# Performance work log

Hardware: AMD Instinct MI355X
Metric: run time of the kernel (lower is better)

The kernel has to match this reference:

```python
import jax, jax.numpy as jnp
import numpy as np

IN_F, OUT_F, USER_F = 1024, 512, 512
BSZ, S = 64, 256


def setup_inputs() -> dict:
    key = jax.random.key(0)
    k = jax.random.split(key, 7)
    X_doc = jax.random.normal(k[0], (BSZ, S, IN_F), dtype=jnp.float32)
    X_user = jax.random.normal(k[1], (BSZ, S, USER_F), dtype=jnp.float32)
    # xavier-normal-ish scaling for weights
    Wd = jax.random.normal(k[2], (OUT_F, IN_F), dtype=jnp.float32) * np.sqrt(2.0 / (IN_F + OUT_F))
    bd = jnp.zeros((OUT_F,), dtype=jnp.float32)
    Wu = jax.random.normal(k[3], (OUT_F, USER_F), dtype=jnp.float32) * np.sqrt(2.0 / (USER_F + OUT_F))
    bu = jnp.zeros((OUT_F,), dtype=jnp.float32)
    W = jax.random.normal(k[4], (OUT_F, OUT_F), dtype=jnp.float32) * np.sqrt(1.0 / OUT_F)
    return {"X_doc": X_doc, "X_user": X_user, "Wd": Wd, "bd": bd, "Wu": Wu, "bu": bu, "W": W}


def reference(X_doc, X_user, Wd, bd, Wu, bu, W):
    d = jnp.einsum('bsi,oi->bso', X_doc, Wd) + bd          # (b, s, out)
    u = jnp.einsum('bsi,oi->bso', X_user, Wu) + bu          # (b, s, out)
    d = d * jax.nn.sigmoid(u)
    u = u * jax.nn.sigmoid(d)
    att = jnp.tanh(jnp.einsum('bsd,de,bre->bsr', d, W, u))  # (b, s, s)
    score_d = jax.nn.softmax(att.mean(axis=2), axis=1)[..., None]  # (b, s, 1)
    score_u = jax.nn.softmax(att.mean(axis=1), axis=1)[..., None]  # (b, s, 1)
    attention_d = jnp.sum(score_d * d, axis=1)              # (b, out)
    attention_u = jnp.sum(score_u * u, axis=1)              # (b, out)
    return (attention_d, attention_u)
```

## Files before the change

### kernel.cpp

```cpp
#include <hip/hip_runtime.h>

#define S_ 256
#define BSZ_ 64
#define IN_F_ 1024
#define OUT_F_ 512
#define USER_F_ 512

typedef short short8 __attribute__((ext_vector_type(8)));
typedef float f32x4 __attribute__((ext_vector_type(4)));

__device__ __forceinline__ ushort f2bf(float f) {
  unsigned u = __float_as_uint(f);
  unsigned r = (u + 0x7FFFu + ((u >> 16) & 1u)) >> 16;
  return (ushort)r;
}
__device__ __forceinline__ float bf2f(unsigned hi16) {
  return __uint_as_float(hi16 << 16);
}
__device__ __forceinline__ float sigf(float x) {
  return 1.f / (1.f + __expf(-x));
}
__device__ __forceinline__ float tanh_safe(float x) {
  float ax = fabsf(x);
  float e = __expf(-2.f * ax);
  float r = (1.f - e) / (1.f + e);
  return copysignf(r, x);
}

__device__ __forceinline__ void gl_lds16(const ushort* g, ushort* l) {
  __builtin_amdgcn_global_load_lds(
      (const __attribute__((address_space(1))) void*)g,
      (__attribute__((address_space(3))) void*)l, 16, 0, 0);
}

__global__ void convert_bf16(const float* __restrict__ in, ushort* __restrict__ out, long n) {
  long i = ((long)blockIdx.x * blockDim.x + threadIdx.x) * 4;
  if (i + 3 < n) {
    float4 v = *(const float4*)(in + i);
    ushort4 o;
    o.x = f2bf(v.x); o.y = f2bf(v.y); o.z = f2bf(v.z); o.w = f2bf(v.w);
    *(ushort4*)(out + i) = o;
  }
}

__global__ void convert_transpose_w(const float* __restrict__ in, ushort* __restrict__ out) {
  int i = blockIdx.x * blockDim.x + threadIdx.x;
  int e = i >> 9, d = i & 511;
  out[i] = f2bf(in[d * 512 + e]);
}

__global__ void zerof(float* __restrict__ p, int n) {
  int i = blockIdx.x * 256 + threadIdx.x;
  if (i < n) p[i] = 0.f;
}

__device__ __forceinline__ void stage_tile(const ushort* __restrict__ g, int K,
                                           ushort* lds, int w, int lane) {
  const int rin = lane >> 3;
  const int c = lane & 7;
#pragma unroll
  for (int i = 0; i < 4; ++i) {
    int r = w * 32 + i * 8 + rin;
    int gc = c ^ (r & 7);
    gl_lds16(g + (long)r * K + gc * 8, lds + w * 2048 + i * 512);
  }
}

__device__ __forceinline__ short8 frag(const ushort* lds, int row, int kk, int q) {
  int pc = (kk * 4 + q) ^ (row & 7);
  return *(const short8*)(lds + row * 64 + pc * 8);
}

__device__ __forceinline__ void compute_step(const ushort* As, const ushort* Bs,
                                             f32x4 acc[4][4], int wr, int wc,
                                             int mlane, int q) {
#pragma unroll
  for (int kk = 0; kk < 2; ++kk) {
    short8 af[4], bfr[4];
#pragma unroll
    for (int r = 0; r < 4; ++r) af[r] = frag(As, wr * 64 + r * 16 + mlane, kk, q);
#pragma unroll
    for (int c = 0; c < 4; ++c) bfr[c] = frag(Bs, wc * 64 + c * 16 + mlane, kk, q);
#pragma unroll
    for (int r = 0; r < 4; ++r)
#pragma unroll
      for (int c = 0; c < 4; ++c)
        acc[r][c] = __builtin_amdgcn_mfma_f32_16x16x32_bf16(af[r], bfr[c], acc[r][c], 0, 0, 0);
  }
}

template <int NSTEP>
__device__ __forceinline__ void gemm_loop(const ushort* __restrict__ A,
                                          const ushort* __restrict__ B, int K,
                                          ushort* As0, ushort* Bs0,
                                          ushort* As1, ushort* Bs1,
                                          f32x4 acc[4][4], int w, int lane,
                                          int wr, int wc, int mlane, int q) {
  stage_tile(A, K, As0, w, lane);
  stage_tile(B, K, Bs0, w, lane);
#pragma unroll 1
  for (int k = 0; k < NSTEP; k += 2) {
    __syncthreads();
    if (k + 1 < NSTEP) {
      stage_tile(A + (k + 1) * 64, K, As1, w, lane);
      stage_tile(B + (k + 1) * 64, K, Bs1, w, lane);
    }
    compute_step(As0, Bs0, acc, wr, wc, mlane, q);
    __syncthreads();
    if (k + 2 < NSTEP) {
      stage_tile(A + (k + 2) * 64, K, As0, w, lane);
      stage_tile(B + (k + 2) * 64, K, Bs0, w, lane);
    }
    if (k + 1 < NSTEP) compute_step(As1, Bs1, acc, wr, wc, mlane, q);
  }
  __syncthreads();
}

#define ACC_ZERO(a)                         \
  _Pragma("unroll") for (int r = 0; r < 4; ++r) \
  _Pragma("unroll") for (int c = 0; c < 4; ++c) { \
    a[r][c][0] = 0.f; a[r][c][1] = 0.f; a[r][c][2] = 0.f; a[r][c][3] = 0.f; }

__global__ __launch_bounds__(256, 2) void gemm_du(
    const ushort* __restrict__ Xd, const ushort* __restrict__ Wd,
    const float* __restrict__ bd,
    const ushort* __restrict__ Xu, const ushort* __restrict__ Wu,
    const float* __restrict__ bu,
    ushort* __restrict__ dg, ushort* __restrict__ ug) {
  __shared__ ushort sm[32768];
  ushort* As0 = sm; ushort* Bs0 = sm + 8192;
  ushort* As1 = sm + 16384; ushort* Bs1 = sm + 24576;
  const int tid = threadIdx.x, lane = tid & 63, w = tid >> 6;
  const int wr = w >> 1, wc = w & 1, mlane = lane & 15, q = lane >> 4;
  const int m0 = blockIdx.y * 128, n0 = blockIdx.x * 128;

  f32x4 accd[4][4]; ACC_ZERO(accd);
  gemm_loop<16>(Xd + (long)m0 * 1024, Wd + (long)n0 * 1024, 1024,
                As0, Bs0, As1, Bs1, accd, w, lane, wr, wc, mlane, q);
  f32x4 accu[4][4]; ACC_ZERO(accu);
  gemm_loop<8>(Xu + (long)m0 * 512, Wu + (long)n0 * 512, 512,
               As0, Bs0, As1, Bs1, accu, w, lane, wr, wc, mlane, q);

#pragma unroll
  for (int c = 0; c < 4; ++c) {
    const int gn = n0 + wc * 64 + c * 16 + mlane;
    const float bdv = bd[gn], buv = bu[gn];
#pragma unroll
    for (int r = 0; r < 4; ++r)
#pragma unroll
      for (int i = 0; i < 4; ++i) {
        const int gm = m0 + wr * 64 + r * 16 + q * 4 + i;
        const long idx = (long)gm * OUT_F_ + gn;
        float dp = accd[r][c][i] + bdv;
        float up = accu[r][c][i] + buv;
        float dgv = dp * sigf(up);
        float ugv = up * sigf(dgv);
        dg[idx] = f2bf(dgv);
        ug[idx] = f2bf(ugv);
      }
  }
}

__global__ __launch_bounds__(256, 2) void gemm_t(
    const ushort* __restrict__ dgp, const ushort* __restrict__ Wt,
    ushort* __restrict__ tout) {
  __shared__ ushort sm[32768];
  ushort* As0 = sm; ushort* Bs0 = sm + 8192;
  ushort* As1 = sm + 16384; ushort* Bs1 = sm + 24576;
  const int tid = threadIdx.x, lane = tid & 63, w = tid >> 6;
  const int wr = w >> 1, wc = w & 1, mlane = lane & 15, q = lane >> 4;
  const int m0 = blockIdx.y * 128, n0 = blockIdx.x * 128;

  f32x4 acc[4][4]; ACC_ZERO(acc);
  gemm_loop<8>(dgp + (long)m0 * 512, Wt + (long)n0 * 512, 512,
               As0, Bs0, As1, Bs1, acc, w, lane, wr, wc, mlane, q);

#pragma unroll
  for (int c = 0; c < 4; ++c) {
    const int gn = n0 + wc * 64 + c * 16 + mlane;
#pragma unroll
    for (int r = 0; r < 4; ++r)
#pragma unroll
      for (int i = 0; i < 4; ++i) {
        const int gm = m0 + wr * 64 + r * 16 + q * 4 + i;
        tout[(long)gm * OUT_F_ + gn] = f2bf(acc[r][c][i]);
      }
  }
}

__global__ __launch_bounds__(256, 2) void gemm_att(
    const ushort* __restrict__ t, const ushort* __restrict__ ug,
    float* __restrict__ rowlog, float* __restrict__ collog) {
  __shared__ ushort sm[32768];
  ushort* As0 = sm; ushort* Bs0 = sm + 8192;
  ushort* As1 = sm + 16384; ushort* Bs1 = sm + 24576;
  const int tid = threadIdx.x, lane = tid & 63, w = tid >> 6;
  const int wr = w >> 1, wc = w & 1, mlane = lane & 15, q = lane >> 4;
  const int b = blockIdx.z;
  const ushort* A = t + (long)b * (S_ * OUT_F_) + (long)blockIdx.y * 128 * 512;
  const ushort* B = ug + (long)b * (S_ * OUT_F_) + (long)blockIdx.x * 128 * 512;

  f32x4 acc[4][4]; ACC_ZERO(acc);
  gemm_loop<8>(A, B, 512, As0, Bs0, As1, Bs1, acc, w, lane, wr, wc, mlane, q);

  float rs[4][4];
  float cs[4];
#pragma unroll
  for (int r = 0; r < 4; ++r)
#pragma unroll
    for (int i = 0; i < 4; ++i) rs[r][i] = 0.f;
#pragma unroll
  for (int c = 0; c < 4; ++c) cs[c] = 0.f;
#pragma unroll
  for (int r = 0; r < 4; ++r)
#pragma unroll
    for (int c = 0; c < 4; ++c)
#pragma unroll
      for (int i = 0; i < 4; ++i) {
        float v = tanh_safe(acc[r][c][i]);
        rs[r][i] += v;
        cs[c] += v;
      }
#pragma unroll
  for (int m = 1; m < 16; m <<= 1)
#pragma unroll
    for (int r = 0; r < 4; ++r)
#pragma unroll
      for (int i = 0; i < 4; ++i) rs[r][i] += __shfl_xor(rs[r][i], m, 64);
#pragma unroll
  for (int m = 16; m < 64; m <<= 1)
#pragma unroll
    for (int c = 0; c < 4; ++c) cs[c] += __shfl_xor(cs[c], m, 64);

  float* rsum = (float*)sm;
  float* csum = ((float*)sm) + 128;
  if (tid < 128) rsum[tid] = 0.f;
  else if (tid < 256) csum[tid - 128] = 0.f;
  __syncthreads();
  if (mlane == 0) {
#pragma unroll
    for (int r = 0; r < 4; ++r)
#pragma unroll
      for (int i = 0; i < 4; ++i)
        atomicAdd(&rsum[wr * 64 + r * 16 + q * 4 + i], rs[r][i]);
  }
  if (q == 0) {
#pragma unroll
    for (int c = 0; c < 4; ++c) atomicAdd(&csum[wc * 64 + c * 16 + mlane], cs[c]);
  }
  __syncthreads();
  if (tid < 128)
    atomicAdd(&rowlog[b * S_ + blockIdx.y * 128 + tid], rsum[tid]);
  else if (tid < 256)
    atomicAdd(&collog[b * S_ + blockIdx.x * 128 + (tid - 128)], csum[tid - 128]);
}

__device__ __forceinline__ float block_max(float v, float* buf, int tid) {
  buf[tid] = v; __syncthreads();
  for (int s = 128; s > 0; s >>= 1) {
    if (tid < s) buf[tid] = fmaxf(buf[tid], buf[tid + s]);
    __syncthreads();
  }
  float r = buf[0]; __syncthreads();
  return r;
}
__device__ __forceinline__ float block_sum(float v, float* buf, int tid) {
  buf[tid] = v; __syncthreads();
  for (int s = 128; s > 0; s >>= 1) {
    if (tid < s) buf[tid] = buf[tid] + buf[tid + s];
    __syncthreads();
  }
  float r = buf[0]; __syncthreads();
  return r;
}

__global__ __launch_bounds__(256) void finalize(
    const float* __restrict__ rowlog, const float* __restrict__ collog,
    const ushort* __restrict__ dg, const ushort* __restrict__ ug,
    float* __restrict__ out) {
  __shared__ float sd[S_], su[S_], buf[S_];
  const int b = blockIdx.x, tid = threadIdx.x;

  const float rowmean = rowlog[b * S_ + tid] * (1.f / (float)S_);
  const float colmean = collog[b * S_ + tid] * (1.f / (float)S_);

  float md = block_max(rowmean, buf, tid);
  float ed = __expf(rowmean - md);
  float sds = block_sum(ed, buf, tid);
  sd[tid] = ed / sds;
  float mu = block_max(colmean, buf, tid);
  float eu = __expf(colmean - mu);
  float sus = block_sum(eu, buf, tid);
  su[tid] = eu / sus;
  __syncthreads();

  const ushort* dgb = dg + (long)b * (S_ * OUT_F_);
  const ushort* ugb = ug + (long)b * (S_ * OUT_F_);
  float ad0 = 0.f, ad1 = 0.f, au0 = 0.f, au1 = 0.f;
  const int o = 2 * tid;
  for (int s = 0; s < S_; ++s) {
    const float wd = sd[s], wu = su[s];
    unsigned dv = *(const unsigned*)(dgb + s * OUT_F_ + o);
    unsigned uv = *(const unsigned*)(ugb + s * OUT_F_ + o);
    ad0 += wd * bf2f(dv & 0xffffu); ad1 += wd * bf2f(dv >> 16);
    au0 += wu * bf2f(uv & 0xffffu); au1 += wu * bf2f(uv >> 16);
  }
  out[b * OUT_F_ + o] = ad0;
  out[b * OUT_F_ + o + 1] = ad1;
  out[BSZ_ * OUT_F_ + b * OUT_F_ + o] = au0;
  out[BSZ_ * OUT_F_ + b * OUT_F_ + o + 1] = au1;
}

extern "C" void kernel_launch(void* const* d_in, const int* in_sizes, int n_in,
                              void* d_out, int out_size, void* d_ws, size_t ws_size,
                              hipStream_t stream) {
  (void)in_sizes; (void)n_in; (void)out_size; (void)ws_size;
  const float* Xd = (const float*)d_in[0];
  const float* Xu = (const float*)d_in[1];
  const float* Wd = (const float*)d_in[2];
  const float* bd = (const float*)d_in[3];
  const float* Wu = (const float*)d_in[4];
  const float* bu = (const float*)d_in[5];
  const float* W  = (const float*)d_in[6];
  float* out = (float*)d_out;
  char* ws = (char*)d_ws;

  ushort* Xd_bf  = (ushort*)(ws + 0L);
  ushort* Xu_bf  = (ushort*)(ws + 33554432L);
  ushort* Wd_bf  = (ushort*)(ws + 50331648L);
  ushort* Wu_bf  = (ushort*)(ws + 51380224L);
  ushort* Wt_bf  = (ushort*)(ws + 51904512L);
  ushort* dg     = (ushort*)(ws + 52428800L);
  ushort* ug     = (ushort*)(ws + 69206016L);
  ushort* t_bf   = (ushort*)(ws + 85983232L);
  float*  rowlog = (float*)(ws + 102760448L);
  float*  collog = (float*)(ws + 102825984L);

  convert_bf16<<<16384, 256, 0, stream>>>(Xd, Xd_bf, 16777216L);
  convert_bf16<<<8192, 256, 0, stream>>>(Xu, Xu_bf, 8388608L);
  convert_bf16<<<512, 256, 0, stream>>>(Wd, Wd_bf, 524288L);
  convert_bf16<<<256, 256, 0, stream>>>(Wu, Wu_bf, 262144L);
  convert_transpose_w<<<1024, 256, 0, stream>>>(W, Wt_bf);
  zerof<<<128, 256, 0, stream>>>(rowlog, 32768);

  dim3 blk(256);
  gemm_du<<<dim3(4, 128), blk, 0, stream>>>(Xd_bf, Wd_bf, bd, Xu_bf, Wu_bf, bu, dg, ug);
  gemm_t<<<dim3(4, 128), blk, 0, stream>>>(dg, Wt_bf, t_bf);
  gemm_att<<<dim3(2, 2, 64), blk, 0, stream>>>(t_bf, ug, rowlog, collog);
  finalize<<<64, 256, 0, stream>>>(rowlog, collog, dg, ug, out);
}
```

Measured before the change: 234.8 us.

## Stage GEMM tiles through registers and remap blocks for XCD locality

Replaces direct global-to-LDS async loads with a register-staged double-buffered pipeline. Each thread loads the next tile into registers while computing the current one, then writes it to swizzled LDS, with a single lgkmcnt wait plus barrier per step. All three GEMM kernels also switch to a 1D grid whose block index is remapped, so blocks sharing A rows (or a batch) land together across the 8 XCDs for better L2 reuse. The register staging raises VGPR pressure under launch_bounds(256,2) and adds an explicit LDS write pass.

After: 400.9 us. 1.71x slower.

```diff
diff --git a/kernel.cpp b/kernel.cpp
--- a/kernel.cpp
+++ b/kernel.cpp
@@ -27,10 +27,9 @@
   return copysignf(r, x);
 }
 
-__device__ __forceinline__ void gl_lds16(const ushort* g, ushort* l) {
-  __builtin_amdgcn_global_load_lds(
-      (const __attribute__((address_space(1))) void*)g,
-      (__attribute__((address_space(3))) void*)l, 16, 0, 0);
+__device__ __forceinline__ void wg_barrier_lds() {
+  asm volatile("s_waitcnt lgkmcnt(0)" ::: "memory");
+  __builtin_amdgcn_s_barrier();
 }
 
 __global__ void convert_bf16(const float* __restrict__ in, ushort* __restrict__ out, long n) {
@@ -54,15 +53,21 @@
   if (i < n) p[i] = 0.f;
 }
 
-__device__ __forceinline__ void stage_tile(const ushort* __restrict__ g, int K,
-                                           ushort* lds, int w, int lane) {
-  const int rin = lane >> 3;
-  const int c = lane & 7;
+struct Stg { uint4 v[4]; };
+
+__device__ __forceinline__ void ld_tile(Stg& s, const ushort* __restrict__ g,
+                                        int K, int t) {
+  const int row = t >> 1, h = t & 1;
+  const uint4* p = (const uint4*)(g + (long)row * K + h * 32);
+  s.v[0] = p[0]; s.v[1] = p[1]; s.v[2] = p[2]; s.v[3] = p[3];
+}
+__device__ __forceinline__ void st_tile(const Stg& s, ushort* lds, int t) {
+  const int row = t >> 1, h = t & 1;
+  ushort* base = lds + row * 64;
 #pragma unroll
   for (int i = 0; i < 4; ++i) {
-    int r = w * 32 + i * 8 + rin;
-    int gc = c ^ (r & 7);
-    gl_lds16(g + (long)r * K + gc * 8, lds + w * 2048 + i * 512);
+    int pc = (h * 4 + i) ^ (row & 7);
+    *(uint4*)(base + pc * 8) = s.v[i];
   }
 }
 
@@ -90,30 +95,36 @@
 }
 
 template <int NSTEP>
-__device__ __forceinline__ void gemm_loop(const ushort* __restrict__ A,
-                                          const ushort* __restrict__ B, int K,
-                                          ushort* As0, ushort* Bs0,
-                                          ushort* As1, ushort* Bs1,
-                                          f32x4 acc[4][4], int w, int lane,
-                                          int wr, int wc, int mlane, int q) {
-  stage_tile(A, K, As0, w, lane);
-  stage_tile(B, K, Bs0, w, lane);
+__device__ __forceinline__ void gemm_loop_rs(const ushort* __restrict__ A,
+                                             const ushort* __restrict__ B, int K,
+                                             ushort* As0, ushort* Bs0,
+                                             ushort* As1, ushort* Bs1,
+                                             f32x4 acc[4][4], int t,
+                                             int wr, int wc, int mlane, int q) {
+  Stg a0, b0, a1, b1;
+  ld_tile(a0, A, K, t); ld_tile(b0, B, K, t);
+  st_tile(a0, As0, t);  st_tile(b0, Bs0, t);
+  ld_tile(a1, A + 64, K, t); ld_tile(b1, B + 64, K, t);
+  wg_barrier_lds();
 #pragma unroll 1
   for (int k = 0; k < NSTEP; k += 2) {
-    __syncthreads();
-    if (k + 1 < NSTEP) {
-      stage_tile(A + (k + 1) * 64, K, As1, w, lane);
-      stage_tile(B + (k + 1) * 64, K, Bs1, w, lane);
+    st_tile(a1, As1, t); st_tile(b1, Bs1, t);
+    if (k + 2 < NSTEP) {
+      ld_tile(a0, A + (k + 2) * 64, K, t);
+      ld_tile(b0, B + (k + 2) * 64, K, t);
     }
     compute_step(As0, Bs0, acc, wr, wc, mlane, q);
-    __syncthreads();
+    wg_barrier_lds();
     if (k + 2 < NSTEP) {
-      stage_tile(A + (k + 2) * 64, K, As0, w, lane);
-      stage_tile(B + (k + 2) * 64, K, Bs0, w, lane);
+      st_tile(a0, As0, t); st_tile(b0, Bs0, t);
+      if (k + 3 < NSTEP) {
+        ld_tile(a1, A + (k + 3) * 64, K, t);
+        ld_tile(b1, B + (k + 3) * 64, K, t);
+      }
     }
-    if (k + 1 < NSTEP) compute_step(As1, Bs1, acc, wr, wc, mlane, q);
-  }
-  __syncthreads();
+    compute_step(As1, Bs1, acc, wr, wc, mlane, q);
+    wg_barrier_lds();
+  }
 }
 
 #define ACC_ZERO(a)                         \
@@ -130,16 +141,19 @@
   __shared__ ushort sm[32768];
   ushort* As0 = sm; ushort* Bs0 = sm + 8192;
   ushort* As1 = sm + 16384; ushort* Bs1 = sm + 24576;
+  const int i = blockIdx.x;
+  const int k8 = i & 7, j = i >> 3;
+  const int by = k8 * 16 + (j >> 2), bx = j & 3;
   const int tid = threadIdx.x, lane = tid & 63, w = tid >> 6;
   const int wr = w >> 1, wc = w & 1, mlane = lane & 15, q = lane >> 4;
-  const int m0 = blockIdx.y * 128, n0 = blockIdx.x * 128;
+  const int m0 = by * 128, n0 = bx * 128;
 
   f32x4 accd[4][4]; ACC_ZERO(accd);
-  gemm_loop<16>(Xd + (long)m0 * 1024, Wd + (long)n0 * 1024, 1024,
-                As0, Bs0, As1, Bs1, accd, w, lane, wr, wc, mlane, q);
+  gemm_loop_rs<16>(Xd + (long)m0 * 1024, Wd + (long)n0 * 1024, 1024,
+                   As0, Bs0, As1, Bs1, accd, tid, wr, wc, mlane, q);
   f32x4 accu[4][4]; ACC_ZERO(accu);
-  gemm_loop<8>(Xu + (long)m0 * 512, Wu + (long)n0 * 512, 512,
-               As0, Bs0, As1, Bs1, accu, w, lane, wr, wc, mlane, q);
+  gemm_loop_rs<8>(Xu + (long)m0 * 512, Wu + (long)n0 * 512, 512,
+                  As0, Bs0, As1, Bs1, accu, tid, wr, wc, mlane, q);
 
 #pragma unroll
   for (int c = 0; c < 4; ++c) {
@@ -148,11 +162,11 @@
 #pragma unroll
     for (int r = 0; r < 4; ++r)
 #pragma unroll
-      for (int i = 0; i < 4; ++i) {
-        const int gm = m0 + wr * 64 + r * 16 + q * 4 + i;
+      for (int ii = 0; ii < 4; ++ii) {
+        const int gm = m0 + wr * 64 + r * 16 + q * 4 + ii;
         const long idx = (long)gm * OUT_F_ + gn;
-        float dp = accd[r][c][i] + bdv;
-        float up = accu[r][c][i] + buv;
+        float dp = accd[r][c][ii] + bdv;
+        float up = accu[r][c][ii] + buv;
         float dgv = dp * sigf(up);
         float ugv = up * sigf(dgv);
         dg[idx] = f2bf(dgv);
@@ -167,13 +181,16 @@
   __shared__ ushort sm[32768];
   ushort* As0 = sm; ushort* Bs0 = sm + 8192;
   ushort* As1 = sm + 16384; ushort* Bs1 = sm + 24576;
+  const int i = blockIdx.x;
+  const int k8 = i & 7, j = i >> 3;
+  const int by = k8 * 16 + (j >> 2), bx = j & 3;
   const int tid = threadIdx.x, lane = tid & 63, w = tid >> 6;
   const int wr = w >> 1, wc = w & 1, mlane = lane & 15, q = lane >> 4;
-  const int m0 = blockIdx.y * 128, n0 = blockIdx.x * 128;
+  const int m0 = by * 128, n0 = bx * 128;
 
   f32x4 acc[4][4]; ACC_ZERO(acc);
-  gemm_loop<8>(dgp + (long)m0 * 512, Wt + (long)n0 * 512, 512,
-               As0, Bs0, As1, Bs1, acc, w, lane, wr, wc, mlane, q);
+  gemm_loop_rs<8>(dgp + (long)m0 * 512, Wt + (long)n0 * 512, 512,
+                  As0, Bs0, As1, Bs1, acc, tid, wr, wc, mlane, q);
 
 #pragma unroll
   for (int c = 0; c < 4; ++c) {
@@ -181,9 +198,9 @@
 #pragma unroll
     for (int r = 0; r < 4; ++r)
 #pragma unroll
-      for (int i = 0; i < 4; ++i) {
-        const int gm = m0 + wr * 64 + r * 16 + q * 4 + i;
-        tout[(long)gm * OUT_F_ + gn] = f2bf(acc[r][c][i]);
+      for (int ii = 0; ii < 4; ++ii) {
+        const int gm = m0 + wr * 64 + r * 16 + q * 4 + ii;
+        tout[(long)gm * OUT_F_ + gn] = f2bf(acc[r][c][ii]);
       }
   }
 }
@@ -194,21 +211,23 @@
   __shared__ ushort sm[32768];
   ushort* As0 = sm; ushort* Bs0 = sm + 8192;
   ushort* As1 = sm + 16384; ushort* Bs1 = sm + 24576;
+  const int i = blockIdx.x;
+  const int k8 = i & 7, j = i >> 3;
+  const int b = k8 * 8 + (j >> 2);
+  const int by = (j >> 1) & 1, bx = j & 1;
   const int tid = threadIdx.x, lane = tid & 63, w = tid >> 6;
   const int wr = w >> 1, wc = w & 1, mlane = lane & 15, q = lane >> 4;
-  const int b = blockIdx.z;
-  const ushort* A = t + (long)b * (S_ * OUT_F_) + (long)blockIdx.y * 128 * 512;
-  const ushort* B = ug + (long)b * (S_ * OUT_F_) + (long)blockIdx.x * 128 * 512;
+  const ushort* A = t + (long)b * (S_ * OUT_F_) + (long)by * 128 * 512;
+  const ushort* B = ug + (long)b * (S_ * OUT_F_) + (long)bx * 128 * 512;
 
   f32x4 acc[4][4]; ACC_ZERO(acc);
-  gemm_loop<8>(A, B, 512, As0, Bs0, As1, Bs1, acc, w, lane, wr, wc, mlane, q);
-
-  float rs[4][4];
-  float cs[4];
+  gemm_loop_rs<8>(A, B, 512, As0, Bs0, As1, Bs1, acc, tid, wr, wc, mlane, q);
+
+  float rs[4][4], cs[4];
 #pragma unroll
   for (int r = 0; r < 4; ++r)
 #pragma unroll
-    for (int i = 0; i < 4; ++i) rs[r][i] = 0.f;
+    for (int ii = 0; ii < 4; ++ii) rs[r][ii] = 0.f;
 #pragma unroll
   for (int c = 0; c < 4; ++c) cs[c] = 0.f;
 #pragma unroll
@@ -216,9 +235,9 @@
 #pragma unroll
     for (int c = 0; c < 4; ++c)
 #pragma unroll
-      for (int i = 0; i < 4; ++i) {
-        float v = tanh_safe(acc[r][c][i]);
-        rs[r][i] += v;
+      for (int ii = 0; ii < 4; ++ii) {
+        float v = tanh_safe(acc[r][c][ii]);
+        rs[r][ii] += v;
         cs[c] += v;
       }
 #pragma unroll
@@ -226,7 +245,7 @@
 #pragma unroll
     for (int r = 0; r < 4; ++r)
 #pragma unroll
-      for (int i = 0; i < 4; ++i) rs[r][i] += __shfl_xor(rs[r][i], m, 64);
+      for (int ii = 0; ii < 4; ++ii) rs[r][ii] += __shfl_xor(rs[r][ii], m, 64);
 #pragma unroll
   for (int m = 16; m < 64; m <<= 1)
 #pragma unroll
@@ -234,6 +253,7 @@
 
   float* rsum = (float*)sm;
   float* csum = ((float*)sm) + 128;
+  __syncthreads();
   if (tid < 128) rsum[tid] = 0.f;
   else if (tid < 256) csum[tid - 128] = 0.f;
   __syncthreads();
@@ -241,8 +261,8 @@
 #pragma unroll
     for (int r = 0; r < 4; ++r)
 #pragma unroll
-      for (int i = 0; i < 4; ++i)
-        atomicAdd(&rsum[wr * 64 + r * 16 + q * 4 + i], rs[r][i]);
+      for (int ii = 0; ii < 4; ++ii)
+        atomicAdd(&rsum[wr * 64 + r * 16 + q * 4 + ii], rs[r][ii]);
   }
   if (q == 0) {
 #pragma unroll
@@ -250,9 +270,9 @@
   }
   __syncthreads();
   if (tid < 128)
-    atomicAdd(&rowlog[b * S_ + blockIdx.y * 128 + tid], rsum[tid]);
+    atomicAdd(&rowlog[b * S_ + by * 128 + tid], rsum[tid]);
   else if (tid < 256)
-    atomicAdd(&collog[b * S_ + blockIdx.x * 128 + (tid - 128)], csum[tid - 128]);
+    atomicAdd(&collog[b * S_ + bx * 128 + (tid - 128)], csum[tid - 128]);
 }
 
 __device__ __forceinline__ float block_max(float v, float* buf, int tid) {
@@ -344,8 +364,8 @@
   zerof<<<128, 256, 0, stream>>>(rowlog, 32768);
 
   dim3 blk(256);
-  gemm_du<<<dim3(4, 128), blk, 0, stream>>>(Xd_bf, Wd_bf, bd, Xu_bf, Wu_bf, bu, dg, ug);
-  gemm_t<<<dim3(4, 128), blk, 0, stream>>>(dg, Wt_bf, t_bf);
-  gemm_att<<<dim3(2, 2, 64), blk, 0, stream>>>(t_bf, ug, rowlog, collog);
+  gemm_du<<<512, blk, 0, stream>>>(Xd_bf, Wd_bf, bd, Xu_bf, Wu_bf, bu, dg, ug);
+  gemm_t<<<512, blk, 0, stream>>>(dg, Wt_bf, t_bf);
+  gemm_att<<<256, blk, 0, stream>>>(t_bf, ug, rowlog, collog);
   finalize<<<64, 256, 0, stream>>>(rowlog, collog, dg, ug, out);
 }
```

## Shrink GEMM tiles to 64x128, drop double buffering, remap blocks for XCD locality

Applied to the files above, without the earlier changes.

All three GEMM kernels now use 64x128 output tiles with single-buffered LDS (24 KB) and launch bounds raised to 4 blocks per CU, so grids grow to 1024/512 blocks. Block indices are remapped so consecutive blocks on the same XCD share M rows or batch, aiming for better L2 reuse. The trade is more occupancy and wave count against lost load/compute overlap inside a block and more redundant B-tile loads.

Measured after the change: 223.6 us. 1.05x faster.

```diff
diff --git a/kernel.cpp b/kernel.cpp
--- a/kernel.cpp
+++ b/kernel.cpp
@@ -54,15 +54,16 @@
   if (i < n) p[i] = 0.f;
 }
 
+template <int ROWS>
 __device__ __forceinline__ void stage_tile(const ushort* __restrict__ g, int K,
                                            ushort* lds, int w, int lane) {
   const int rin = lane >> 3;
   const int c = lane & 7;
 #pragma unroll
-  for (int i = 0; i < 4; ++i) {
-    int r = w * 32 + i * 8 + rin;
+  for (int i = 0; i < ROWS / 32; ++i) {
+    int r = w * (ROWS / 4) + i * 8 + rin;
     int gc = c ^ (r & 7);
-    gl_lds16(g + (long)r * K + gc * 8, lds + w * 2048 + i * 512);
+    gl_lds16(g + (long)r * K + gc * 8, lds + w * (ROWS / 4) * 64 + i * 512);
   }
 }
 
@@ -72,17 +73,17 @@
 }
 
 __device__ __forceinline__ void compute_step(const ushort* As, const ushort* Bs,
-                                             f32x4 acc[4][4], int wr, int wc,
+                                             f32x4 acc[2][4], int wr, int wc,
                                              int mlane, int q) {
 #pragma unroll
   for (int kk = 0; kk < 2; ++kk) {
-    short8 af[4], bfr[4];
-#pragma unroll
-    for (int r = 0; r < 4; ++r) af[r] = frag(As, wr * 64 + r * 16 + mlane, kk, q);
+    short8 af[2], bfr[4];
+#pragma unroll
+    for (int r = 0; r < 2; ++r) af[r] = frag(As, wr * 32 + r * 16 + mlane, kk, q);
 #pragma unroll
     for (int c = 0; c < 4; ++c) bfr[c] = frag(Bs, wc * 64 + c * 16 + mlane, kk, q);
 #pragma unroll
-    for (int r = 0; r < 4; ++r)
+    for (int r = 0; r < 2; ++r)
 #pragma unroll
       for (int c = 0; c < 4; ++c)
         acc[r][c] = __builtin_amdgcn_mfma_f32_16x16x32_bf16(af[r], bfr[c], acc[r][c], 0, 0, 0);
@@ -92,67 +93,58 @@
 template <int NSTEP>
 __device__ __forceinline__ void gemm_loop(const ushort* __restrict__ A,
                                           const ushort* __restrict__ B, int K,
-                                          ushort* As0, ushort* Bs0,
-                                          ushort* As1, ushort* Bs1,
-                                          f32x4 acc[4][4], int w, int lane,
-                                          int wr, int wc, int mlane, int q) {
-  stage_tile(A, K, As0, w, lane);
-  stage_tile(B, K, Bs0, w, lane);
+                                          ushort* As, ushort* Bs, f32x4 acc[2][4],
+                                          int w, int lane, int wr, int wc,
+                                          int mlane, int q) {
 #pragma unroll 1
-  for (int k = 0; k < NSTEP; k += 2) {
+  for (int k = 0; k < NSTEP; ++k) {
+    stage_tile<64>(A + k * 64, K, As, w, lane);
+    stage_tile<128>(B + k * 64, K, Bs, w, lane);
     __syncthreads();
-    if (k + 1 < NSTEP) {
-      stage_tile(A + (k + 1) * 64, K, As1, w, lane);
-      stage_tile(B + (k + 1) * 64, K, Bs1, w, lane);
-    }
-    compute_step(As0, Bs0, acc, wr, wc, mlane, q);
+    compute_step(As, Bs, acc, wr, wc, mlane, q);
     __syncthreads();
-    if (k + 2 < NSTEP) {
-      stage_tile(A + (k + 2) * 64, K, As0, w, lane);
-      stage_tile(B + (k + 2) * 64, K, Bs0, w, lane);
-    }
-    if (k + 1 < NSTEP) compute_step(As1, Bs1, acc, wr, wc, mlane, q);
-  }
-  __syncthreads();
-}
-
-#define ACC_ZERO(a)                         \
-  _Pragma("unroll") for (int r = 0; r < 4; ++r) \
+  }
+}
+
+#define ACC_ZERO(a)                             \
+  _Pragma("unroll") for (int r = 0; r < 2; ++r) \
   _Pragma("unroll") for (int c = 0; c < 4; ++c) { \
     a[r][c][0] = 0.f; a[r][c][1] = 0.f; a[r][c][2] = 0.f; a[r][c][3] = 0.f; }
 
-__global__ __launch_bounds__(256, 2) void gemm_du(
+__global__ __launch_bounds__(256, 4) void gemm_du(
     const ushort* __restrict__ Xd, const ushort* __restrict__ Wd,
     const float* __restrict__ bd,
     const ushort* __restrict__ Xu, const ushort* __restrict__ Wu,
     const float* __restrict__ bu,
     ushort* __restrict__ dg, ushort* __restrict__ ug) {
-  __shared__ ushort sm[32768];
-  ushort* As0 = sm; ushort* Bs0 = sm + 8192;
-  ushort* As1 = sm + 16384; ushort* Bs1 = sm + 24576;
+  __shared__ ushort sm[12288];
+  ushort* As = sm; ushort* Bs = sm + 4096;
+  const int i = blockIdx.x;
+  const int k8 = i & 7, j = i >> 3;
+  const int by = k8 * 32 + (j >> 2), bx = j & 3;
   const int tid = threadIdx.x, lane = tid & 63, w = tid >> 6;
   const int wr = w >> 1, wc = w & 1, mlane = lane & 15, q = lane >> 4;
-  const int m0 = blockIdx.y * 128, n0 = blockIdx.x * 128;
-
-  f32x4 accd[4][4]; ACC_ZERO(accd);
+  const int m0 = by * 64, n0 = bx * 128;
+
+  f32x4 accd[2][4]; ACC_ZERO(accd);
   gemm_loop<16>(Xd + (long)m0 * 1024, Wd + (long)n0 * 1024, 1024,
-                As0, Bs0, As1, Bs1, accd, w, lane, wr, wc, mlane, q);
-  f32x4 accu[4][4]; ACC_ZERO(accu);
+                As, Bs, accd, w, lane, wr, wc, mlane, q);
+  f32x4 accu[2][4]; ACC_ZERO(accu);
   gemm_loop<8>(Xu + (long)m0 * 512, Wu + (long)n0 * 512, 512,
-               As0, Bs0, As1, Bs1, accu, w, lane, wr, wc, mlane, q);
+               As, Bs, accu, w, lane, wr, wc, mlane, q);
 
 #pragma unroll
   for (int c = 0; c < 4; ++c) {
     const int gn = n0 + wc * 64 + c * 16 + mlane;
     const float bdv = bd[gn], buv = bu[gn];
 #pragma unroll
-    for (int r = 0; r < 4; ++r)
-#pragma unroll
-      for (int i = 0; i < 4; ++i) {
-        const int gm = m0 + wr * 64 + r * 16 + q * 4 + i;
+    for (int r = 0; r < 2; ++r)
+#pragma unroll
+      for (int ii = 0; ii < 4; ++ii) {
+        const int gm = m0 + wr * 32 + r * 16 + q * 4 + ii;
         const long idx = (long)gm * OUT_F_ + gn;
-        float dp = accd[r][c][i] + bdv;
-        float up = accu[r][c][i] + buv;
+        float dp = accd[r][c][ii] + bdv;
+        float up = accu[r][c][ii] + buv;
         float dgv = dp * sigf(up);
         float ugv = up * sigf(dgv);
         dg[idx] = f2bf(dgv);
@@ -161,98 +153,101 @@
   }
 }
 
-__global__ __launch_bounds__(256, 2) void gemm_t(
+__global__ __launch_bounds__(256, 4) void gemm_t(
     const ushort* __restrict__ dgp, const ushort* __restrict__ Wt,
     ushort* __restrict__ tout) {
-  __shared__ ushort sm[32768];
-  ushort* As0 = sm; ushort* Bs0 = sm + 8192;
-  ushort* As1 = sm + 16384; ushort* Bs1 = sm + 24576;
+  __shared__ ushort sm[12288];
+  ushort* As = sm; ushort* Bs = sm + 4096;
+  const int i = blockIdx.x;
+  const int k8 = i & 7, j = i >> 3;
+  const int by = k8 * 32 + (j >> 2), bx = j & 3;
   const int tid = threadIdx.x, lane = tid & 63, w = tid >> 6;
   const int wr = w >> 1, wc = w & 1, mlane = lane & 15, q = lane >> 4;
-  const int m0 = blockIdx.y * 128, n0 = blockIdx.x * 128;
-
-  f32x4 acc[4][4]; ACC_ZERO(acc);
+  const int m0 = by * 64, n0 = bx * 128;
+
+  f32x4 acc[2][4]; ACC_ZERO(acc);
   gemm_loop<8>(dgp + (long)m0 * 512, Wt + (long)n0 * 512, 512,
-               As0, Bs0, As1, Bs1, acc, w, lane, wr, wc, mlane, q);
+               As, Bs, acc, w, lane, wr, wc, mlane, q);
 
 #pragma unroll
   for (int c = 0; c < 4; ++c) {
     const int gn = n0 + wc * 64 + c * 16 + mlane;
 #pragma unroll
-    for (int r = 0; r < 4; ++r)
-#pragma unroll
-      for (int i = 0; i < 4; ++i) {
-        const int gm = m0 + wr * 64 + r * 16 + q * 4 + i;
-        tout[(long)gm * OUT_F_ + gn] = f2bf(acc[r][c][i]);
+    for (int r = 0; r < 2; ++r)
+#pragma unroll
+      for (int ii = 0; ii < 4; ++ii) {
+        const int gm = m0 + wr * 32 + r * 16 + q * 4 + ii;
+        tout[(long)gm * OUT_F_ + gn] = f2bf(acc[r][c][ii]);
       }
   }
 }
 
-__global__ __launch_bounds__(256, 2) void gemm_att(
+__global__ __launch_bounds__(256, 4) void gemm_att(
     const ushort* __restrict__ t, const ushort* __restrict__ ug,
     float* __restrict__ rowlog, float* __restrict__ collog) {
-  __shared__ ushort sm[32768];
-  ushort* As0 = sm; ushort* Bs0 = sm + 8192;
-  ushort* As1 = sm + 16384; ushort* Bs1 = sm + 24576;
+  __shared__ ushort sm[12288];
+  ushort* As = sm; ushort* Bs = sm + 4096;
+  const int i = blockIdx.x;
+  const int k8 = i & 7, j = i >> 3;
+  const int b = k8 * 8 + (j >> 3);
+  const int l = j & 7, by = l >> 1, bx = l & 1;
   const int tid = threadIdx.x, lane = tid & 63, w = tid >> 6;
   const int wr = w >> 1, wc = w & 1, mlane = lane & 15, q = lane >> 4;
-  const int b = blockIdx.z;
-  const ushort* A = t + (long)b * (S_ * OUT_F_) + (long)blockIdx.y * 128 * 512;
-  const ushort* B = ug + (long)b * (S_ * OUT_F_) + (long)blockIdx.x * 128 * 512;
-
-  f32x4 acc[4][4]; ACC_ZERO(acc);
-  gemm_loop<8>(A, B, 512, As0, Bs0, As1, Bs1, acc, w, lane, wr, wc, mlane, q);
-
-  float rs[4][4];
-  float cs[4];
-#pragma unroll
-  for (int r = 0; r < 4; ++r)
-#pragma unroll
-    for (int i = 0; i < 4; ++i) rs[r][i] = 0.f;
+  const ushort* A = t + (long)b * (S_ * OUT_F_) + (long)by * 64 * 512;
+  const ushort* B = ug + (long)b * (S_ * OUT_F_) + (long)bx * 128 * 512;
+
+  f32x4 acc[2][4]; ACC_ZERO(acc);
+  gemm_loop<8>(A, B, 512, As, Bs, acc, w, lane, wr, wc, mlane, q);
+
+  float rs[2][4], cs[4];
+#pragma unroll
+  for (int r = 0; r < 2; ++r)
+#pragma unroll
+    for (int ii = 0; ii < 4; ++ii) rs[r][ii] = 0.f;
 #pragma unroll
   for (int c = 0; c < 4; ++c) cs[c] = 0.f;
 #pragma unroll
-  for (int r = 0; r < 4; ++r)
+  for (int r = 0; r < 2; ++r)
 #pragma unroll
     for (int c = 0; c < 4; ++c)
 #pragma unroll
-      for (int i = 0; i < 4; ++i) {
-        float v = tanh_safe(acc[r][c][i]);
-        rs[r][i] += v;
+      for (int ii = 0; ii < 4; ++ii) {
+        float v = tanh_safe(acc[r][c][ii]);
+        rs[r][ii] += v;
         cs[c] += v;
       }
 #pragma unroll
   for (int m = 1; m < 16; m <<= 1)
 #pragma unroll
-    for (int r = 0; r < 4; ++r)
-#pragma unroll
-      for (int i = 0; i < 4; ++i) rs[r][i] += __shfl_xor(rs[r][i], m, 64);
+    for (int r = 0; r < 2; ++r)
+#pragma unroll
+      for (int ii = 0; ii < 4; ++ii) rs[r][ii] += __shfl_xor(rs[r][ii], m, 64);
 #pragma unroll
   for (int m = 16; m < 64; m <<= 1)
 #pragma unroll
     for (int c = 0; c < 4; ++c) cs[c] += __shfl_xor(cs[c], m, 64);
 
   float* rsum = (float*)sm;
-  float* csum = ((float*)sm) + 128;
-  if (tid < 128) rsum[tid] = 0.f;
-  else if (tid < 256) csum[tid - 128] = 0.f;
+  float* csum = ((float*)sm) + 64;
+  if (tid < 64) rsum[tid] = 0.f;
+  else if (tid < 192) csum[tid - 64] = 0.f;
   __syncthreads();
   if (mlane == 0) {
 #pragma unroll
-    for (int r = 0; r < 4; ++r)
-#pragma unroll
-      for (int i = 0; i < 4; ++i)
-        atomicAdd(&rsum[wr * 64 + r * 16 + q * 4 + i], rs[r][i]);
+    for (int r = 0; r < 2; ++r)
+#pragma unroll
+      for (int ii = 0; ii < 4; ++ii)
+        atomicAdd(&rsum[wr * 32 + r * 16 + q * 4 + ii], rs[r][ii]);
   }
   if (q == 0) {
 #pragma unroll
     for (int c = 0; c < 4; ++c) atomicAdd(&csum[wc * 64 + c * 16 + mlane], cs[c]);
   }
   __syncthreads();
-  if (tid < 128)
-    atomicAdd(&rowlog[b * S_ + blockIdx.y * 128 + tid], rsum[tid]);
-  else if (tid < 256)
-    atomicAdd(&collog[b * S_ + blockIdx.x * 128 + (tid - 128)], csum[tid - 128]);
+  if (tid < 64)
+    atomicAdd(&rowlog[b * S_ + by * 64 + tid], rsum[tid]);
+  else if (tid < 192)
+    atomicAdd(&collog[b * S_ + bx * 128 + (tid - 64)], csum[tid - 64]);
 }
 
 __device__ __forceinline__ float block_max(float v, float* buf, int tid) {
@@ -344,8 +339,8 @@
   zerof<<<128, 256, 0, stream>>>(rowlog, 32768);
 
   dim3 blk(256);
-  gemm_du<<<dim3(4, 128), blk, 0, stream>>>(Xd_bf, Wd_bf, bd, Xu_bf, Wu_bf, bu, dg, ug);
-  gemm_t<<<dim3(4, 128), blk, 0, stream>>>(dg, Wt_bf, t_bf);
-  gemm_att<<<dim3(2, 2, 64), blk, 0, stream>>>(t_bf, ug, rowlog, collog);
+  gemm_du<<<1024, blk, 0, stream>>>(Xd_bf, Wd_bf, bd, Xu_bf, Wu_bf, bu, dg, ug);
+  gemm_t<<<1024, blk, 0, stream>>>(dg, Wt_bf, t_bf);
+  gemm_att<<<512, blk, 0, stream>>>(t_bf, ug, rowlog, collog);
   finalize<<<64, 256, 0, stream>>>(rowlog, collog, dg, ug, out);
 }
```
